# Kernel optimization log

Measured on AMD Instinct MI355X. Metric: run time of the kernel, lower is better.

Reference implementation:

```python
import jax, jax.numpy as jnp
import numpy as np
import math

NUM_HEADS = 16
D_MODEL = 1024
LN_EPS = 1e-5


def _layer_norm(x, g, b):
    mu = jnp.mean(x, axis=-1, keepdims=True)
    var = jnp.mean((x - mu) ** 2, axis=-1, keepdims=True)
    return (x - mu) / jnp.sqrt(var + LN_EPS) * g + b


def setup_inputs() -> dict:
    key = jax.random.key(0)
    ks = jax.random.split(key, 12)
    B, H, W, d = 32, 16, 16, D_MODEL
    P, F = 64, 128
    s = 0.02
    return {
        "x": jax.random.normal(ks[0], (B, H, W, d), jnp.float32),
        "pattern_features": jax.random.normal(ks[1], (B, P, F), jnp.float32),
        "wq": jax.random.normal(ks[2], (d, d), jnp.float32) * s,
        "bq": jnp.zeros((d,), jnp.float32),
        "wk": jax.random.normal(ks[3], (d, d), jnp.float32) * s,
        "bk": jnp.zeros((d,), jnp.float32),
        "wv": jax.random.normal(ks[4], (d, d), jnp.float32) * s,
        "bv": jnp.zeros((d,), jnp.float32),
        "wo": jax.random.normal(ks[5], (d, d), jnp.float32) * s,
        "bo": jnp.zeros((d,), jnp.float32),
        "ln_g": jnp.ones((d,), jnp.float32),
        "ln_b": jnp.zeros((d,), jnp.float32),
    }


def reference(x, pattern_features, wq, bq, wk, bk, wv, bv, wo, bo, ln_g, ln_b):
    B, H, W, d = x.shape
    S = H * W
    nh = NUM_HEADS
    dk = d // nh
    x_seq = x.reshape(B, S, d)

    def proj(w, b):
        return (x_seq @ w.T + b).reshape(B, S, nh, dk).transpose(0, 2, 1, 3)  # (B,nh,S,dk)

    q, k, v = proj(wq, bq), proj(wk, bk), proj(wv, bv)
    scores = jnp.einsum("bhsd,bhtd->bhst", q, k) / math.sqrt(dk)  # (B,nh,S,S)

    # creative bias: diversity bonus on top-left min(S,64) block, same for all heads
    m = min(S, 64)
    sim = jnp.einsum("bpf,bqf->bpq", pattern_features, pattern_features)
    div = 1.0 - jax.nn.softmax(sim, axis=-1)  # (B,P,P)
    bias = jnp.zeros((B, nh, S, S), x.dtype)
    bias = bias.at[:, :, :m, :m].set(div[:, None, :m, :m] * 0.1)

    # faithful to torch: scores + bias.unsqueeze(0) -> rank-5 (1,B,nh,S,S)
    scores5 = scores[None] + bias[None]
    aw = jax.nn.softmax(scores5, axis=-1)
    attn = jnp.matmul(aw, v)  # (1,B,nh,S,dk) via broadcasting
    # faithful to torch transpose(1,2).view(B,S,d): row-major reshape of (1,nh,B,S,dk)
    attn = jnp.transpose(attn, (0, 2, 1, 3, 4)).reshape(B, S, d)

    out = attn @ wo.T + bo
    out = _layer_norm(out + x_seq, ln_g, ln_b)

    attention_weights = jax.nn.softmax(scores, axis=-1).mean(axis=1)  # (B,S,S)
    return out.reshape(B, H, W, d), attention_weights
```

## Files before the change

### kernel.cpp

```cpp
#include <hip/hip_runtime.h>

typedef unsigned short u16;
typedef unsigned int   u32;
typedef short bf16x8 __attribute__((ext_vector_type(8)));
typedef float f32x4  __attribute__((ext_vector_type(4)));

__device__ __forceinline__ float bf2f(u16 u){
  union { u32 u; float f; } c; c.u = ((u32)u) << 16; return c.f;
}
__device__ __forceinline__ u16 f2bf(float f){
  union { float f; u32 u; } c; c.f = f;
  u32 u = c.u + 0x7fffu + ((c.u >> 16) & 1u);
  return (u16)(u >> 16);
}

__device__ __forceinline__ void gload16(const u16* g, u16* l){
  __builtin_amdgcn_global_load_lds((const __attribute__((address_space(1))) u32*)g,
                                   (__attribute__((address_space(3))) u32*)l, 16, 0, 0);
}

__device__ __forceinline__ float waveRed(float v, int ismax){
  #pragma unroll
  for (int o = 32; o > 0; o >>= 1){
    float t = __shfl_xor(v, o, 64);
    v = ismax ? fmaxf(v, t) : (v + t);
  }
  return v;
}
__device__ __forceinline__ float blockRed(float v, int ismax, float* red, int tid){
  v = waveRed(v, ismax);
  __syncthreads();
  if ((tid & 63) == 0) red[tid >> 6] = v;
  __syncthreads();
  return ismax ? fmaxf(fmaxf(red[0], red[1]), fmaxf(red[2], red[3]))
               : (red[0] + red[1] + red[2] + red[3]);
}

__global__ __launch_bounds__(256)
void conv_x(const float* __restrict__ src, u16* __restrict__ dst){
  const size_t i = ((size_t)blockIdx.x * 256 + threadIdx.x) * 8;
  const float4 a = *(const float4*)(src + i);
  const float4 b = *(const float4*)(src + i + 4);
  uint4 o;
  o.x = (u32)f2bf(a.x) | ((u32)f2bf(a.y) << 16);
  o.y = (u32)f2bf(a.z) | ((u32)f2bf(a.w) << 16);
  o.z = (u32)f2bf(b.x) | ((u32)f2bf(b.y) << 16);
  o.w = (u32)f2bf(b.z) | ((u32)f2bf(b.w) << 16);
  *(uint4*)(dst + i) = o;
}

__global__ __launch_bounds__(256)
void conv_w4(const float* __restrict__ w0, const float* __restrict__ w1,
             const float* __restrict__ w2, const float* __restrict__ w3,
             u16* __restrict__ dst){
  const float* s = blockIdx.y == 0 ? w0 : (blockIdx.y == 1 ? w1 : (blockIdx.y == 2 ? w2 : w3));
  u16* d = dst + (size_t)blockIdx.y * 1048576;
  const size_t i = ((size_t)blockIdx.x * 256 + threadIdx.x) * 8;
  const float4 a = *(const float4*)(s + i);
  const float4 b = *(const float4*)(s + i + 4);
  uint4 o;
  o.x = (u32)f2bf(a.x) | ((u32)f2bf(a.y) << 16);
  o.y = (u32)f2bf(a.z) | ((u32)f2bf(a.w) << 16);
  o.z = (u32)f2bf(b.x) | ((u32)f2bf(b.y) << 16);
  o.w = (u32)f2bf(b.z) | ((u32)f2bf(b.w) << 16);
  *(uint4*)(d + i) = o;
}

__global__ __launch_bounds__(256)
void div_kernel(const float* __restrict__ pf, float* __restrict__ divp)
{
  __shared__ float pfs[64][129];
  __shared__ float svs[64][65];
  const int b = blockIdx.x;
  const int tid = threadIdx.x;
  const float* pb = pf + (size_t)b * 8192;
  for (int i = tid; i < 8192; i += 256) pfs[i >> 7][i & 127] = pb[i];
  __syncthreads();
  const int p = tid & 63, qg = tid >> 6;
  for (int qq = qg * 16; qq < qg * 16 + 16; ++qq){
    float a = 0.f;
    #pragma unroll 8
    for (int f = 0; f < 128; ++f) a += pfs[p][f] * pfs[qq][f];
    svs[p][qq] = a;
  }
  __syncthreads();
  if (tid < 64){
    float m = -1e30f;
    for (int qq = 0; qq < 64; ++qq) m = fmaxf(m, svs[tid][qq]);
    float s = 0.f;
    for (int qq = 0; qq < 64; ++qq){ const float e = __expf(svs[tid][qq] - m); svs[tid][qq] = e; s += e; }
    const float inv = 1.f / s;
    float* dr = divp + ((size_t)b * 64 + tid) * 64;
    for (int qq = 0; qq < 64; ++qq) dr[qq] = 0.1f * (1.f - svs[tid][qq] * inv);
  }
}

template<int MODE>
__global__ __launch_bounds__(256, 3)
void gemm_lds(const u16* __restrict__ A, const u16* __restrict__ Wb,
              const float* __restrict__ bias0, const float* __restrict__ bias1,
              const float* __restrict__ bias2, void* __restrict__ outp)
{
  __shared__ u16 As[3][4096];
  __shared__ u16 Bs[3][4096];
  const int tid = threadIdx.x, lane = tid & 63, w = tid >> 6;
  const int wm = (w >> 1) * 64, wn = (w & 1) * 64;
  const int bm = blockIdx.x;
  int bn = blockIdx.y;
  const u16* Wp = Wb;
  const float* bias = bias0;
  float scale = 1.f;
  int wsel = 0;
  if (MODE == 0){
    wsel = bn >> 3; bn &= 7;
    Wp = Wb + (size_t)wsel * 1048576;
    bias = wsel == 0 ? bias0 : (wsel == 1 ? bias1 : bias2);
    if (wsel == 0) scale = 0.125f;
  }

  const f32x4 z = {0.f, 0.f, 0.f, 0.f};
  f32x4 acc[4][4];
  #pragma unroll
  for (int i = 0; i < 4; ++i)
    #pragma unroll
    for (int j = 0; j < 4; ++j) acc[i][j] = z;

  const int r4  = lane >> 2;
  const int c8s = (((lane & 3) ^ ((lane >> 3) & 3)) * 8);
  const int ca0 = w * 2, ca1 = w * 2 + 1;
  const u16* gA0 = A  + (size_t)(bm * 128 + ca0 * 16 + r4) * 1024 + c8s;
  const u16* gA1 = A  + (size_t)(bm * 128 + ca1 * 16 + r4) * 1024 + c8s;
  const u16* gB0 = Wp + (size_t)(bn * 128 + ca0 * 16 + r4) * 1024 + c8s;
  const u16* gB1 = Wp + (size_t)(bn * 128 + ca1 * 16 + r4) * 1024 + c8s;
  const int lo0 = ca0 * 512 + lane * 8;
  const int lo1 = ca1 * 512 + lane * 8;

  const int fr = lane & 15, quad = lane >> 4;
  int offA[4], offB[4];
  #pragma unroll
  for (int i = 0; i < 4; ++i){
    const int r = wm + i * 16 + fr;
    offA[i] = r * 32 + ((quad ^ ((r >> 1) & 3)) * 8);
  }
  #pragma unroll
  for (int j = 0; j < 4; ++j){
    const int r = wn + j * 16 + fr;
    offB[j] = r * 32 + ((quad ^ ((r >> 1) & 3)) * 8);
  }

#define STG(s, kk) \
    gload16(gA0 + (kk), &As[s][lo0]); \
    gload16(gA1 + (kk), &As[s][lo1]); \
    gload16(gB0 + (kk), &Bs[s][lo0]); \
    gload16(gB1 + (kk), &Bs[s][lo1]);

  STG(0, 0)
  STG(1, 32)
  asm volatile("s_waitcnt vmcnt(4)" ::: "memory");
  __builtin_amdgcn_sched_barrier(0);
  __builtin_amdgcn_s_barrier();
  asm volatile("" ::: "memory");
  __builtin_amdgcn_sched_barrier(0);

  int slot = 0;
  #pragma unroll 1
  for (int t = 0; t < 32; ++t){
    const int s2 = slot < 1 ? 2 : slot - 1;
    if (t < 30){ STG(s2, (t + 2) * 32) }
    const u16* as_ = As[slot];
    const u16* bs_ = Bs[slot];
    bf16x8 af[4], bfv[4];
    #pragma unroll
    for (int i = 0; i < 4; ++i) af[i]  = *(const bf16x8*)&as_[offA[i]];
    #pragma unroll
    for (int j = 0; j < 4; ++j) bfv[j] = *(const bf16x8*)&bs_[offB[j]];
    __builtin_amdgcn_s_setprio(1);
    #pragma unroll
    for (int i = 0; i < 4; ++i)
      #pragma unroll
      for (int j = 0; j < 4; ++j)
        acc[i][j] = __builtin_amdgcn_mfma_f32_16x16x32_bf16(af[i], bfv[j], acc[i][j], 0, 0, 0);
    __builtin_amdgcn_s_setprio(0);
    if (t < 30)       { asm volatile("s_waitcnt vmcnt(4)" ::: "memory"); }
    else if (t == 30) { asm volatile("s_waitcnt vmcnt(0)" ::: "memory"); }
    if (t < 31){
      __builtin_amdgcn_sched_barrier(0);
      __builtin_amdgcn_s_barrier();
      asm volatile("" ::: "memory");
      __builtin_amdgcn_sched_barrier(0);
    }
    slot = slot == 2 ? 0 : slot + 1;
  }
#undef STG

  #pragma unroll
  for (int i = 0; i < 4; ++i){
    #pragma unroll
    for (int j = 0; j < 4; ++j){
      const int gr0 = bm * 128 + wm + i * 16 + ((lane >> 4) * 4);
      const int gc  = bn * 128 + wn + j * 16 + (lane & 15);
      const float bvv = bias[gc];
      #pragma unroll
      for (int r = 0; r < 4; ++r){
        const int gr = gr0 + r;
        const float val = (acc[i][j][r] + bvv) * scale;
        if (MODE == 0){
          const int b = gr >> 8, s = gr & 255, h = gc >> 6, kk = gc & 63;
          ((u16*)outp)[(size_t)wsel * 8388608 + (size_t)b * 262144 +
                       (size_t)h * 16384 + (size_t)s * 64 + kk] = f2bf(val);
        } else {
          ((float*)outp)[(size_t)gr * 1024 + gc] = val;
        }
      }
    }
  }
}

__global__ __launch_bounds__(256)
void attn_mfma(const u16* __restrict__ q, const u16* __restrict__ k,
               const u16* __restrict__ v, const float* __restrict__ divp,
               u16* __restrict__ attn_s)
{
  __shared__ u16 Vt[64][264];
  __shared__ u16 Ps[4][16][136];
  const int bh = blockIdx.x;
  const int b = bh >> 4, h = bh & 15;
  const int tid = threadIdx.x, lane = tid & 63, w = tid >> 6;
  const int quad = lane >> 4, l15 = lane & 15;
  const u16* kh = k + (size_t)bh * 16384;
  const u16* vh = v + (size_t)bh * 16384;
  const u16* qh = q + (size_t)bh * 16384;

  #pragma unroll
  for (int c = 0; c < 4; ++c){
    const int pidx = tid + c * 256;
    const int t2 = pidx & 127;
    const int n0 = (pidx >> 7) * 8;
    const uint4 a  = *(const uint4*)(vh + (2 * t2) * 64 + n0);
    const uint4 bb = *(const uint4*)(vh + (2 * t2 + 1) * 64 + n0);
    const u32 aa[4] = {a.x, a.y, a.z, a.w};
    const u32 bb4[4] = {bb.x, bb.y, bb.z, bb.w};
    #pragma unroll
    for (int j2 = 0; j2 < 4; ++j2){
      const u32 lo = aa[j2], hi = bb4[j2];
      *(u32*)&Vt[n0 + 2 * j2    ][2 * t2] = (lo & 0xffffu) | (hi << 16);
      *(u32*)&Vt[n0 + 2 * j2 + 1][2 * t2] = (lo >> 16) | (hi & 0xffff0000u);
    }
  }
  __syncthreads();

  const f32x4 z = {0.f, 0.f, 0.f, 0.f};
  const int bp = 2 * h + (b >> 4);
  for (int i = 0; i < 4; ++i){
    const int row0 = w * 64 + i * 16;
    const bf16x8 af0 = *(const bf16x8*)(qh + (size_t)(row0 + l15) * 64 + quad * 8);
    const bf16x8 af1 = *(const bf16x8*)(qh + (size_t)(row0 + l15) * 64 + 32 + quad * 8);
    f32x4 sc[16];
    #pragma unroll
    for (int ct = 0; ct < 16; ++ct){
      const bf16x8 b0 = *(const bf16x8*)(kh + (size_t)(ct * 16 + l15) * 64 + quad * 8);
      const bf16x8 b1 = *(const bf16x8*)(kh + (size_t)(ct * 16 + l15) * 64 + 32 + quad * 8);
      f32x4 a = __builtin_amdgcn_mfma_f32_16x16x32_bf16(af0, b0, z, 0, 0, 0);
      sc[ct]  = __builtin_amdgcn_mfma_f32_16x16x32_bf16(af1, b1, a, 0, 0, 0);
    }
    if (w == 0){
      const float* dv = divp + (size_t)b * 4096 + (size_t)(i * 16 + quad * 4) * 64 + l15;
      #pragma unroll
      for (int ct = 0; ct < 4; ++ct)
        #pragma unroll
        for (int rr = 0; rr < 4; ++rr)
          sc[ct][rr] += dv[rr * 64 + ct * 16];
    }
    float rs[4];
    #pragma unroll
    for (int rr = 0; rr < 4; ++rr){
      float m = sc[0][rr];
      #pragma unroll
      for (int ct = 1; ct < 16; ++ct) m = fmaxf(m, sc[ct][rr]);
      #pragma unroll
      for (int o = 1; o < 16; o <<= 1) m = fmaxf(m, __shfl_xor(m, o, 64));
      float s = 0.f;
      #pragma unroll
      for (int ct = 0; ct < 16; ++ct){
        const float e = __expf(sc[ct][rr] - m); sc[ct][rr] = e; s += e;
      }
      #pragma unroll
      for (int o = 1; o < 16; o <<= 1) s += __shfl_xor(s, o, 64);
      rs[rr] = 1.f / s;
    }
    f32x4 o4[4] = {z, z, z, z};
    #pragma unroll
    for (int half = 0; half < 2; ++half){
      #pragma unroll
      for (int ct = 0; ct < 8; ++ct)
        #pragma unroll
        for (int rr = 0; rr < 4; ++rr)
          Ps[w][quad * 4 + rr][ct * 16 + l15] = f2bf(sc[half * 8 + ct][rr] * rs[rr]);
      #pragma unroll
      for (int kc = 0; kc < 4; ++kc){
        const bf16x8 pa = *(const bf16x8*)&Ps[w][l15][kc * 32 + quad * 8];
        #pragma unroll
        for (int nt = 0; nt < 4; ++nt){
          const bf16x8 vb8 = *(const bf16x8*)&Vt[nt * 16 + l15][half * 128 + kc * 32 + quad * 8];
          o4[nt] = __builtin_amdgcn_mfma_f32_16x16x32_bf16(pa, vb8, o4[nt], 0, 0, 0);
        }
      }
    }
    const int sp = (b & 15) * 16 + (w * 4 + i);
    #pragma unroll
    for (int nt = 0; nt < 4; ++nt)
      #pragma unroll
      for (int rr = 0; rr < 4; ++rr){
        const int slo = quad * 4 + rr;
        const int cp = slo * 64 + nt * 16 + l15;
        attn_s[((size_t)bp * 256 + sp) * 1024 + cp] = f2bf(o4[nt][rr]);
      }
  }
}

__global__ __launch_bounds__(256)
void aw_kernel(const u16* __restrict__ q, const u16* __restrict__ k,
               float* __restrict__ aw)
{
  __shared__ float redm[16][4];
  __shared__ float reds[16][4];
  const int blk = blockIdx.x;
  const int b = blk >> 4, st = blk & 15;
  const int tid = threadIdx.x, lane = tid & 63, w = tid >> 6;
  const int quad = lane >> 4, l15 = lane & 15;
  const int rowb = st * 16;
  const f32x4 z = {0.f, 0.f, 0.f, 0.f};
  float awacc[4][4] = {};
  for (int h = 0; h < 16; ++h){
    const u16* kh = k + (((size_t)b * 16 + h) * 16384);
    const u16* qh = q + (((size_t)b * 16 + h) * 16384);
    const bf16x8 af0 = *(const bf16x8*)(qh + (size_t)(rowb + l15) * 64 + quad * 8);
    const bf16x8 af1 = *(const bf16x8*)(qh + (size_t)(rowb + l15) * 64 + 32 + quad * 8);
    f32x4 sc[4];
    #pragma unroll
    for (int j4 = 0; j4 < 4; ++j4){
      const int ct = w * 4 + j4;
      const bf16x8 b0 = *(const bf16x8*)(kh + (size_t)(ct * 16 + l15) * 64 + quad * 8);
      const bf16x8 b1 = *(const bf16x8*)(kh + (size_t)(ct * 16 + l15) * 64 + 32 + quad * 8);
      f32x4 a = __builtin_amdgcn_mfma_f32_16x16x32_bf16(af0, b0, z, 0, 0, 0);
      sc[j4]  = __builtin_amdgcn_mfma_f32_16x16x32_bf16(af1, b1, a, 0, 0, 0);
    }
    float pm[4];
    #pragma unroll
    for (int rr = 0; rr < 4; ++rr){
      float m = fmaxf(fmaxf(sc[0][rr], sc[1][rr]), fmaxf(sc[2][rr], sc[3][rr]));
      #pragma unroll
      for (int o = 1; o < 16; o <<= 1) m = fmaxf(m, __shfl_xor(m, o, 64));
      pm[rr] = m;
    }
    if (l15 == 0)
      #pragma unroll
      for (int rr = 0; rr < 4; ++rr) redm[quad * 4 + rr][w] = pm[rr];
    __syncthreads();
    float ps[4];
    #pragma unroll
    for (int rr = 0; rr < 4; ++rr){
      const int row = quad * 4 + rr;
      const float m = fmaxf(fmaxf(redm[row][0], redm[row][1]),
                            fmaxf(redm[row][2], redm[row][3]));
      float s = 0.f;
      #pragma unroll
      for (int j4 = 0; j4 < 4; ++j4){
        const float e = __expf(sc[j4][rr] - m); sc[j4][rr] = e; s += e;
      }
      #pragma unroll
      for (int o = 1; o < 16; o <<= 1) s += __shfl_xor(s, o, 64);
      ps[rr] = s;
    }
    if (l15 == 0)
      #pragma unroll
      for (int rr = 0; rr < 4; ++rr) reds[quad * 4 + rr][w] = ps[rr];
    __syncthreads();
    #pragma unroll
    for (int rr = 0; rr < 4; ++rr){
      const int row = quad * 4 + rr;
      const float inv = 1.f / (reds[row][0] + reds[row][1] + reds[row][2] + reds[row][3]);
      #pragma unroll
      for (int j4 = 0; j4 < 4; ++j4) awacc[j4][rr] += sc[j4][rr] * inv;
    }
  }
  const size_t base = (size_t)b * 65536;
  #pragma unroll
  for (int j4 = 0; j4 < 4; ++j4){
    const int col = (w * 4 + j4) * 16 + l15;
    #pragma unroll
    for (int rr = 0; rr < 4; ++rr){
      const int row = rowb + quad * 4 + rr;
      aw[base + (size_t)row * 256 + col] = awacc[j4][rr] * 0.0625f;
    }
  }
}

__global__ __launch_bounds__(256)
void ln_kernel(const float* __restrict__ y2, const float* __restrict__ x,
               const float* __restrict__ g, const float* __restrict__ bb,
               float* __restrict__ outp)
{
  __shared__ float red[4];
  const int r = blockIdx.x, tid = threadIdx.x;
  const float4 yv = ((const float4*)(y2 + (size_t)r * 1024))[tid];
  const float4 xv = ((const float4*)(x  + (size_t)r * 1024))[tid];
  const float v0 = yv.x + xv.x;
  const float v1 = yv.y + xv.y;
  const float v2 = yv.z + xv.z;
  const float v3 = yv.w + xv.w;
  const float ssum = blockRed(v0 + v1 + v2 + v3, 0, red, tid);
  const float mu = ssum * (1.f / 1024.f);
  const float d0 = v0 - mu, d1 = v1 - mu, d2 = v2 - mu, d3 = v3 - mu;
  const float sq = blockRed(d0 * d0 + d1 * d1 + d2 * d2 + d3 * d3, 0, red, tid);
  const float rstd = rsqrtf(sq * (1.f / 1024.f) + 1e-5f);
  const float4 gv = ((const float4*)g)[tid];
  const float4 bv = ((const float4*)bb)[tid];
  float4 o;
  o.x = d0 * rstd * gv.x + bv.x;
  o.y = d1 * rstd * gv.y + bv.y;
  o.z = d2 * rstd * gv.z + bv.z;
  o.w = d3 * rstd * gv.w + bv.w;
  ((float4*)(outp + (size_t)r * 1024))[tid] = o;
}

extern "C" void kernel_launch(void* const* d_in, const int* in_sizes, int n_in,
                              void* d_out, int out_size, void* d_ws, size_t ws_size,
                              hipStream_t stream)
{
  int ix = -1, ipf = -1, iw[4] = {-1,-1,-1,-1}, iv[6] = {-1,-1,-1,-1,-1,-1};
  int nw = 0, nv = 0;
  for (int i = 0; i < n_in; ++i){
    const int sz = in_sizes[i];
    if (sz == 8388608 && ix < 0) ix = i;
    else if (sz == 262144 && ipf < 0) ipf = i;
    else if (sz == 1048576 && nw < 4) iw[nw++] = i;
    else if (sz == 1024 && nv < 6) iv[nv++] = i;
  }
  if (ix < 0 || ipf < 0 || nw != 4 || nv != 6){
    ix = 0; ipf = 1; iw[0] = 2; iv[0] = 3; iw[1] = 4; iv[1] = 5;
    iw[2] = 6; iv[2] = 7; iw[3] = 8; iv[3] = 9; iv[4] = 10; iv[5] = 11;
  }

  const float* x   = (const float*)d_in[ix];
  const float* pf  = (const float*)d_in[ipf];
  const float* wq  = (const float*)d_in[iw[0]];
  const float* wk  = (const float*)d_in[iw[1]];
  const float* wv  = (const float*)d_in[iw[2]];
  const float* wo  = (const float*)d_in[iw[3]];
  const float* bq  = (const float*)d_in[iv[0]];
  const float* bk  = (const float*)d_in[iv[1]];
  const float* bv  = (const float*)d_in[iv[2]];
  const float* bo  = (const float*)d_in[iv[3]];
  const float* lng = (const float*)d_in[iv[4]];
  const float* lnb = (const float*)d_in[iv[5]];

  float* out0   = (float*)d_out;
  float* aw_out = out0 + 8388608;

  u16* x_bf = (u16*)d_out;
  u16* attn = x_bf + 8388608;
  u16* qkv    = (u16*)d_ws;
  float* divp = (float*)((char*)d_ws + (size_t)48 * 1048576);
  u16* warena = (u16*)((char*)d_ws + (size_t)49 * 1048576);
  float* y2   = (float*)d_ws;

  conv_x<<<4096, 256, 0, stream>>>(x, x_bf);
  conv_w4<<<dim3(512, 4), 256, 0, stream>>>(wq, wk, wv, wo, warena);
  div_kernel<<<32, 256, 0, stream>>>(pf, divp);

  gemm_lds<0><<<dim3(64, 24), 256, 0, stream>>>(x_bf, warena, bq, bk, bv, (void*)qkv);

  u16* qw = qkv, *kw = qkv + 8388608, *vw = qkv + 16777216;
  attn_mfma<<<512, 256, 0, stream>>>(qw, kw, vw, divp, attn);
  aw_kernel<<<512, 256, 0, stream>>>(qw, kw, aw_out);

  gemm_lds<1><<<dim3(64, 8), 256, 0, stream>>>(attn, warena + 3145728, bo, nullptr, nullptr, (void*)y2);
  ln_kernel<<<8192, 256, 0, stream>>>(y2, x, lng, lnb, out0);
}
```

Before: 330.2 us.

## Merge conversion kernels, store V transposed, restructure aw kernel per-wave heads

Combines the x and weight bf16 conversion kernels into one launch. The QKV GEMM now writes V already transposed with packed 4-element stores, so the attention kernel reads V^T straight from global memory and no longer stages and transposes it in LDS. The attention-weights kernel gives each wave whole heads over all 256 columns, which removes the per-head block-level max/sum reductions and barriers. Per-wave partial sums are then reduced through LDS into coalesced float4 stores. The cost is higher register pressure (16x4 accumulators) and V fragments fetched from global rather than LDS.

```diff
diff --git a/kernel.cpp b/kernel.cpp
--- a/kernel.cpp
+++ b/kernel.cpp
@@ -37,25 +37,24 @@
 }
 
 __global__ __launch_bounds__(256)
-void conv_x(const float* __restrict__ src, u16* __restrict__ dst){
-  const size_t i = ((size_t)blockIdx.x * 256 + threadIdx.x) * 8;
-  const float4 a = *(const float4*)(src + i);
-  const float4 b = *(const float4*)(src + i + 4);
-  uint4 o;
-  o.x = (u32)f2bf(a.x) | ((u32)f2bf(a.y) << 16);
-  o.y = (u32)f2bf(a.z) | ((u32)f2bf(a.w) << 16);
-  o.z = (u32)f2bf(b.x) | ((u32)f2bf(b.y) << 16);
-  o.w = (u32)f2bf(b.z) | ((u32)f2bf(b.w) << 16);
-  *(uint4*)(dst + i) = o;
-}
-
-__global__ __launch_bounds__(256)
-void conv_w4(const float* __restrict__ w0, const float* __restrict__ w1,
-             const float* __restrict__ w2, const float* __restrict__ w3,
-             u16* __restrict__ dst){
-  const float* s = blockIdx.y == 0 ? w0 : (blockIdx.y == 1 ? w1 : (blockIdx.y == 2 ? w2 : w3));
-  u16* d = dst + (size_t)blockIdx.y * 1048576;
-  const size_t i = ((size_t)blockIdx.x * 256 + threadIdx.x) * 8;
+void conv_all(const float* __restrict__ x, const float* __restrict__ w0,
+              const float* __restrict__ w1, const float* __restrict__ w2,
+              const float* __restrict__ w3, u16* __restrict__ xdst,
+              u16* __restrict__ wdst){
+  const int bid = blockIdx.x;
+  const float* s;
+  u16* d;
+  size_t i;
+  if (bid < 4096){
+    s = x; d = xdst;
+    i = ((size_t)bid * 256 + threadIdx.x) * 8;
+  } else {
+    const int wb = bid - 4096;
+    const int wi = wb >> 9;
+    s = wi == 0 ? w0 : (wi == 1 ? w1 : (wi == 2 ? w2 : w3));
+    d = wdst + (size_t)wi * 1048576;
+    i = ((size_t)(wb & 511) * 256 + threadIdx.x) * 8;
+  }
   const float4 a = *(const float4*)(s + i);
   const float4 b = *(const float4*)(s + i + 4);
   uint4 o;
@@ -197,19 +196,30 @@
   for (int i = 0; i < 4; ++i){
     #pragma unroll
     for (int j = 0; j < 4; ++j){
-      const int gr0 = bm * 128 + wm + i * 16 + ((lane >> 4) * 4);
-      const int gc  = bn * 128 + wn + j * 16 + (lane & 15);
+      const int gr0 = bm * 128 + wm + i * 16 + quad * 4;
+      const int gc  = bn * 128 + wn + j * 16 + fr;
       const float bvv = bias[gc];
-      #pragma unroll
-      for (int r = 0; r < 4; ++r){
-        const int gr = gr0 + r;
-        const float val = (acc[i][j][r] + bvv) * scale;
-        if (MODE == 0){
-          const int b = gr >> 8, s = gr & 255, h = gc >> 6, kk = gc & 63;
-          ((u16*)outp)[(size_t)wsel * 8388608 + (size_t)b * 262144 +
-                       (size_t)h * 16384 + (size_t)s * 64 + kk] = f2bf(val);
-        } else {
-          ((float*)outp)[(size_t)gr * 1024 + gc] = val;
+      if (MODE == 0 && wsel == 2){
+        const int b = gr0 >> 8, s0 = gr0 & 255, h = gc >> 6, kk = gc & 63;
+        const u32 p0 = (u32)f2bf(acc[i][j][0] + bvv) |
+                       ((u32)f2bf(acc[i][j][1] + bvv) << 16);
+        const u32 p1 = (u32)f2bf(acc[i][j][2] + bvv) |
+                       ((u32)f2bf(acc[i][j][3] + bvv) << 16);
+        uint2 pk; pk.x = p0; pk.y = p1;
+        *(uint2*)((u16*)outp + (size_t)2 * 8388608 + (size_t)b * 262144 +
+                  (size_t)h * 16384 + (size_t)kk * 256 + s0) = pk;
+      } else {
+        #pragma unroll
+        for (int r = 0; r < 4; ++r){
+          const int gr = gr0 + r;
+          const float val = (acc[i][j][r] + bvv) * scale;
+          if (MODE == 0){
+            const int b = gr >> 8, s = gr & 255, h = gc >> 6, kk = gc & 63;
+            ((u16*)outp)[(size_t)wsel * 8388608 + (size_t)b * 262144 +
+                         (size_t)h * 16384 + (size_t)s * 64 + kk] = f2bf(val);
+          } else {
+            ((float*)outp)[(size_t)gr * 1024 + gc] = val;
+          }
         }
       }
     }
@@ -218,36 +228,17 @@
 
 __global__ __launch_bounds__(256)
 void attn_mfma(const u16* __restrict__ q, const u16* __restrict__ k,
-               const u16* __restrict__ v, const float* __restrict__ divp,
+               const u16* __restrict__ vT, const float* __restrict__ divp,
                u16* __restrict__ attn_s)
 {
-  __shared__ u16 Vt[64][264];
   __shared__ u16 Ps[4][16][136];
   const int bh = blockIdx.x;
   const int b = bh >> 4, h = bh & 15;
   const int tid = threadIdx.x, lane = tid & 63, w = tid >> 6;
   const int quad = lane >> 4, l15 = lane & 15;
-  const u16* kh = k + (size_t)bh * 16384;
-  const u16* vh = v + (size_t)bh * 16384;
-  const u16* qh = q + (size_t)bh * 16384;
-
-  #pragma unroll
-  for (int c = 0; c < 4; ++c){
-    const int pidx = tid + c * 256;
-    const int t2 = pidx & 127;
-    const int n0 = (pidx >> 7) * 8;
-    const uint4 a  = *(const uint4*)(vh + (2 * t2) * 64 + n0);
-    const uint4 bb = *(const uint4*)(vh + (2 * t2 + 1) * 64 + n0);
-    const u32 aa[4] = {a.x, a.y, a.z, a.w};
-    const u32 bb4[4] = {bb.x, bb.y, bb.z, bb.w};
-    #pragma unroll
-    for (int j2 = 0; j2 < 4; ++j2){
-      const u32 lo = aa[j2], hi = bb4[j2];
-      *(u32*)&Vt[n0 + 2 * j2    ][2 * t2] = (lo & 0xffffu) | (hi << 16);
-      *(u32*)&Vt[n0 + 2 * j2 + 1][2 * t2] = (lo >> 16) | (hi & 0xffff0000u);
-    }
-  }
-  __syncthreads();
+  const u16* kh = k  + (size_t)bh * 16384;
+  const u16* vh = vT + (size_t)bh * 16384;
+  const u16* qh = q  + (size_t)bh * 16384;
 
   const f32x4 z = {0.f, 0.f, 0.f, 0.f};
   const int bp = 2 * h + (b >> 4);
@@ -301,7 +292,8 @@
         const bf16x8 pa = *(const bf16x8*)&Ps[w][l15][kc * 32 + quad * 8];
         #pragma unroll
         for (int nt = 0; nt < 4; ++nt){
-          const bf16x8 vb8 = *(const bf16x8*)&Vt[nt * 16 + l15][half * 128 + kc * 32 + quad * 8];
+          const bf16x8 vb8 = *(const bf16x8*)(vh + (size_t)(nt * 16 + l15) * 256 +
+                                              half * 128 + kc * 32 + quad * 8);
           o4[nt] = __builtin_amdgcn_mfma_f32_16x16x32_bf16(pa, vb8, o4[nt], 0, 0, 0);
         }
       }
@@ -322,77 +314,69 @@
 void aw_kernel(const u16* __restrict__ q, const u16* __restrict__ k,
                float* __restrict__ aw)
 {
-  __shared__ float redm[16][4];
-  __shared__ float reds[16][4];
+  __shared__ __align__(16) float awl[4][16][260];
   const int blk = blockIdx.x;
   const int b = blk >> 4, st = blk & 15;
   const int tid = threadIdx.x, lane = tid & 63, w = tid >> 6;
   const int quad = lane >> 4, l15 = lane & 15;
   const int rowb = st * 16;
   const f32x4 z = {0.f, 0.f, 0.f, 0.f};
-  float awacc[4][4] = {};
-  for (int h = 0; h < 16; ++h){
+  float awacc[16][4] = {};
+  #pragma unroll 1
+  for (int hi = 0; hi < 4; ++hi){
+    const int h = hi * 4 + w;
     const u16* kh = k + (((size_t)b * 16 + h) * 16384);
     const u16* qh = q + (((size_t)b * 16 + h) * 16384);
     const bf16x8 af0 = *(const bf16x8*)(qh + (size_t)(rowb + l15) * 64 + quad * 8);
     const bf16x8 af1 = *(const bf16x8*)(qh + (size_t)(rowb + l15) * 64 + 32 + quad * 8);
-    f32x4 sc[4];
-    #pragma unroll
-    for (int j4 = 0; j4 < 4; ++j4){
-      const int ct = w * 4 + j4;
+    f32x4 sc[16];
+    #pragma unroll
+    for (int ct = 0; ct < 16; ++ct){
       const bf16x8 b0 = *(const bf16x8*)(kh + (size_t)(ct * 16 + l15) * 64 + quad * 8);
       const bf16x8 b1 = *(const bf16x8*)(kh + (size_t)(ct * 16 + l15) * 64 + 32 + quad * 8);
       f32x4 a = __builtin_amdgcn_mfma_f32_16x16x32_bf16(af0, b0, z, 0, 0, 0);
-      sc[j4]  = __builtin_amdgcn_mfma_f32_16x16x32_bf16(af1, b1, a, 0, 0, 0);
-    }
-    float pm[4];
+      sc[ct]  = __builtin_amdgcn_mfma_f32_16x16x32_bf16(af1, b1, a, 0, 0, 0);
+    }
     #pragma unroll
     for (int rr = 0; rr < 4; ++rr){
-      float m = fmaxf(fmaxf(sc[0][rr], sc[1][rr]), fmaxf(sc[2][rr], sc[3][rr]));
+      float m = sc[0][rr];
+      #pragma unroll
+      for (int ct = 1; ct < 16; ++ct) m = fmaxf(m, sc[ct][rr]);
       #pragma unroll
       for (int o = 1; o < 16; o <<= 1) m = fmaxf(m, __shfl_xor(m, o, 64));
-      pm[rr] = m;
-    }
-    if (l15 == 0)
-      #pragma unroll
-      for (int rr = 0; rr < 4; ++rr) redm[quad * 4 + rr][w] = pm[rr];
-    __syncthreads();
-    float ps[4];
-    #pragma unroll
-    for (int rr = 0; rr < 4; ++rr){
-      const int row = quad * 4 + rr;
-      const float m = fmaxf(fmaxf(redm[row][0], redm[row][1]),
-                            fmaxf(redm[row][2], redm[row][3]));
       float s = 0.f;
       #pragma unroll
-      for (int j4 = 0; j4 < 4; ++j4){
-        const float e = __expf(sc[j4][rr] - m); sc[j4][rr] = e; s += e;
+      for (int ct = 0; ct < 16; ++ct){
+        const float e = __expf(sc[ct][rr] - m); sc[ct][rr] = e; s += e;
       }
       #pragma unroll
       for (int o = 1; o < 16; o <<= 1) s += __shfl_xor(s, o, 64);
-      ps[rr] = s;
-    }
-    if (l15 == 0)
-      #pragma unroll
-      for (int rr = 0; rr < 4; ++rr) reds[quad * 4 + rr][w] = ps[rr];
-    __syncthreads();
-    #pragma unroll
-    for (int rr = 0; rr < 4; ++rr){
-      const int row = quad * 4 + rr;
-      const float inv = 1.f / (reds[row][0] + reds[row][1] + reds[row][2] + reds[row][3]);
-      #pragma unroll
-      for (int j4 = 0; j4 < 4; ++j4) awacc[j4][rr] += sc[j4][rr] * inv;
-    }
-  }
-  const size_t base = (size_t)b * 65536;
-  #pragma unroll
-  for (int j4 = 0; j4 < 4; ++j4){
-    const int col = (w * 4 + j4) * 16 + l15;
-    #pragma unroll
-    for (int rr = 0; rr < 4; ++rr){
-      const int row = rowb + quad * 4 + rr;
-      aw[base + (size_t)row * 256 + col] = awacc[j4][rr] * 0.0625f;
-    }
+      const float inv = 1.f / s;
+      #pragma unroll
+      for (int ct = 0; ct < 16; ++ct) awacc[ct][rr] += sc[ct][rr] * inv;
+    }
+  }
+  #pragma unroll
+  for (int ct = 0; ct < 16; ++ct)
+    #pragma unroll
+    for (int rr = 0; rr < 4; ++rr)
+      awl[w][quad * 4 + rr][ct * 16 + l15] = awacc[ct][rr];
+  __syncthreads();
+  const size_t base = (size_t)b * 65536 + (size_t)rowb * 256;
+  #pragma unroll
+  for (int cc = 0; cc < 4; ++cc){
+    const int idx = cc * 1024 + tid * 4;
+    const int row = idx >> 8, col = idx & 255;
+    const float4 a0 = *(const float4*)&awl[0][row][col];
+    const float4 a1 = *(const float4*)&awl[1][row][col];
+    const float4 a2 = *(const float4*)&awl[2][row][col];
+    const float4 a3 = *(const float4*)&awl[3][row][col];
+    float4 o;
+    o.x = (a0.x + a1.x + a2.x + a3.x) * 0.0625f;
+    o.y = (a0.y + a1.y + a2.y + a3.y) * 0.0625f;
+    o.z = (a0.z + a1.z + a2.z + a3.z) * 0.0625f;
+    o.w = (a0.w + a1.w + a2.w + a3.w) * 0.0625f;
+    *(float4*)(aw + base + idx) = o;
   }
 }
 
@@ -465,8 +449,7 @@
   u16* warena = (u16*)((char*)d_ws + (size_t)49 * 1048576);
   float* y2   = (float*)d_ws;
 
-  conv_x<<<4096, 256, 0, stream>>>(x, x_bf);
-  conv_w4<<<dim3(512, 4), 256, 0, stream>>>(wq, wk, wv, wo, warena);
+  conv_all<<<6144, 256, 0, stream>>>(x, wq, wk, wv, wo, x_bf, warena);
   div_kernel<<<32, 256, 0, stream>>>(pf, divp);
 
   gemm_lds<0><<<dim3(64, 24), 256, 0, stream>>>(x_bf, warena, bq, bk, bv, (void*)qkv);
```

After: 339.1 us. 2.7% more time.
